# Performance work log

Hardware: AMD Instinct MI355X
Metric: run time of the kernel (lower is better)

Reference implementation:

```python
import jax, jax.numpy as jnp
import numpy as np

B, C, H, W = 16, 256, 128, 128  # ration = 1 -> C' = C


def setup_inputs() -> dict:
    key = jax.random.key(0)
    ks = jax.random.split(key, 7)
    s = 1.0 / np.sqrt(C)
    return {
        "x": jax.random.normal(ks[0], (B, C, H, W), dtype=jnp.float32),
        "Wq": jax.random.normal(ks[1], (C, C), dtype=jnp.float32) * s,
        "Wk": jax.random.normal(ks[2], (C, C), dtype=jnp.float32) * s,
        "Wv": jax.random.normal(ks[3], (C, C), dtype=jnp.float32) * s,
        "gamma": jax.random.normal(ks[4], (1,), dtype=jnp.float32) * 0.1,
        "Wup": jax.random.normal(ks[5], (C, C), dtype=jnp.float32) * s,
        "b_up": jax.random.normal(ks[6], (C,), dtype=jnp.float32) * 0.01,
    }


def reference(x, Wq, Wk, Wv, gamma, Wup, b_up):
    b, c, h, w = x.shape
    # 1x1 conv (no bias) == channel-mixing einsum, followed by ReLU
    proj = lambda Wm: jax.nn.relu(jnp.einsum('oc,bchw->bohw', Wm, x))
    # torch .view(B, H, -1) is a raw row-major reinterpretation of [B,C,H,W]
    q = proj(Wq).reshape(b, h, -1)                      # [B, H, C*W]
    k = proj(Wk).reshape(b, h, -1).transpose(0, 2, 1)   # [B, C*W, H]
    v = proj(Wv).reshape(b, h, -1).transpose(0, 2, 1)   # [B, C*W, H]
    # non-standard softmax over dim=1 (rows of the HxH score matrix)
    attn = jax.nn.softmax(jnp.matmul(q, k), axis=1)     # [B, H, H]
    out1 = jnp.matmul(v, attn)                          # [B, C*W, H]
    out_h = out1.reshape(b, c, h, w) * gamma            # raw reshape, gamma scale
    # layer_up: 1x1 conv with bias
    out_h = jnp.einsum('oc,bchw->bohw', Wup, out_h) + b_up[None, :, None, None]
    return (out_h, q, k, v, gamma, attn)
```

## Files before the change

kernel.cpp:

```cpp
#include <hip/hip_runtime.h>
#include <stdint.h>


typedef _Float16 f16;
typedef __attribute__((ext_vector_type(8))) _Float16 f16x8;
typedef __attribute__((ext_vector_type(4))) float f32x4;

#define DEV static __device__ __forceinline__

constexpr int  HW   = 16384;
constexpr long PB   = 4194304;
constexpr long HALF = 2097152;

constexpr long WH_OFF  = 0;
constexpr long WL_OFF  = 393216;
constexpr long WU_OFF  = 786432;
constexpr long WS_NEED = 1048576;

DEV unsigned pk2(float a, float b) {
  auto h = __builtin_amdgcn_cvt_pkrtz(a, b);
  return __builtin_bit_cast(unsigned, h);
}
DEV void split_pk2(float a, float b, unsigned& hu, unsigned& lu) {
  auto h = __builtin_amdgcn_cvt_pkrtz(a, b);
  auto l = __builtin_amdgcn_cvt_pkrtz(a - (float)h[0], b - (float)h[1]);
  hu = __builtin_bit_cast(unsigned, h);
  lu = __builtin_bit_cast(unsigned, l);
}
DEV f32x4 mfma16(f16x8 a, f16x8 b, f32x4 c) {
  return __builtin_amdgcn_mfma_f32_16x16x32_f16(a, b, c, 0, 0, 0);
}
DEV f16x8 ld64(const char* base, int row, int g) {
  return *(const f16x8*)(base + row * 64 + 16 * (g ^ ((row >> 1) & 3)));
}

DEV void gload16(const void* g, void* l) {
  __builtin_amdgcn_global_load_lds(
      (const __attribute__((address_space(1))) uint32_t*)(g),
      (__attribute__((address_space(3))) uint32_t*)(l), 16, 0, 0);
}

DEV int swz(int row, int kbyte) {
  return (kbyte & ~63) | ((kbyte & 63) ^ (((row >> 3) & 3) << 4));
}
DEV f16x8 ldfrag(const f16* arr, int strideB, int row, int kbyte) {
  return *(const f16x8*)((const char*)arr + row * strideB + swz(row, kbyte));
}

__global__ __launch_bounds__(256) void prep_w(
    const float* __restrict__ Wq, const float* __restrict__ Wk,
    const float* __restrict__ Wv, const float* __restrict__ Wu,
    const float* __restrict__ gin, char* __restrict__ ws) {
  const int kc = blockIdx.x, m = blockIdx.y, o = threadIdx.x;
  const float* src = (m == 0) ? Wq : (m == 1) ? Wk : (m == 2) ? Wv : Wu;
  const float sc = (m == 3) ? gin[0] : 1.0f;
  float v[32];
#pragma unroll
  for (int j = 0; j < 32; ++j) v[j] = src[o * 256 + kc * 32 + j] * sc;
  char* dh = (m < 3) ? (ws + WH_OFF + ((long)(m * 8 + kc) * 256 + o) * 64)
                     : (ws + WU_OFF + ((long)kc * 256 + o) * 64);
  char* dl = ws + WL_OFF + ((long)(m * 8 + kc) * 256 + o) * 64;
  const int sw = (o >> 1) & 3;
#pragma unroll
  for (int gq = 0; gq < 4; ++gq) {
    unsigned h[4], l[4];
#pragma unroll
    for (int p = 0; p < 4; ++p)
      split_pk2(v[8 * gq + 2 * p], v[8 * gq + 2 * p + 1], h[p], l[p]);
    const int off = 16 * (gq ^ sw);
    *(uint4*)(dh + off) = make_uint4(h[0], h[1], h[2], h[3]);
    if (m < 3) *(uint4*)(dl + off) = make_uint4(l[0], l[1], l[2], l[3]);
  }
}

__global__ __launch_bounds__(256, 2) void qkv_fused3(
    const float* __restrict__ x,
    const char* __restrict__ wqh, const char* __restrict__ wql,
    const char* __restrict__ wkh, const char* __restrict__ wkl,
    const char* __restrict__ wvh,
    float* __restrict__ qseg, float* __restrict__ kseg,
    float* __restrict__ vseg) {
  __shared__ char lds[65536];
  char* Xh = lds;
  char* Xl = lds + 32768;
  float* R = (float*)(lds + 32768);
  const int t = threadIdx.x, lane = t & 63, w = t >> 6;
  const int l15 = lane & 15, g = lane >> 4;
  const int b = blockIdx.y, hw0 = blockIdx.x * 64;
  const float* xb = x + (long)b * PB + hw0;

  {
    const int hw = t & 63, cq = t >> 6;
    const int sw = (hw >> 1) & 3;
#pragma unroll
    for (int j8 = 0; j8 < 8; ++j8) {
      const int c0 = cq * 64 + j8 * 8;
      float v[8];
#pragma unroll
      for (int i = 0; i < 8; ++i) v[i] = xb[(long)(c0 + i) * HW + hw];
      unsigned h[4], l[4];
#pragma unroll
      for (int p = 0; p < 4; ++p)
        split_pk2(v[2 * p], v[2 * p + 1], h[p], l[p]);
      const int kc = c0 >> 5, gi = (c0 >> 3) & 3;
      const int off = kc * 4096 + hw * 64 + 16 * (gi ^ sw);
      *(uint4*)(Xh + off) = make_uint4(h[0], h[1], h[2], h[3]);
      *(uint4*)(Xl + off) = make_uint4(l[0], l[1], l[2], l[3]);
    }
  }
  __syncthreads();

  auto repack_store = [&](f32x4 (&ac)[4][4], float* ob) {
#pragma unroll
    for (int half = 0; half < 2; ++half) {
#pragma unroll
      for (int mf2 = 0; mf2 < 2; ++mf2) {
        const int mf = 2 * half + mf2;
#pragma unroll
        for (int nf = 0; nf < 4; ++nf)
#pragma unroll
          for (int r = 0; r < 4; ++r) {
            const int hwloc = 16 * mf2 + 4 * g + r;
            const int o = w * 64 + 16 * nf + l15;
            const int col = (o >> 1) ^ (((hwloc >> 2) & 3) << 3);
            float v = ac[mf][nf][r];
            R[(o & 1) * 4096 + hwloc * 128 + col] = v > 0.f ? v : 0.f;
          }
      }
      __syncthreads();
#pragma unroll
      for (int it = 0; it < 8; ++it) {
        const int f = t + 256 * it;
        const int parity = f >> 10, hwloc = (f >> 5) & 31, q4 = f & 31;
        const int col = (4 * q4) ^ (((hwloc >> 2) & 3) << 3);
        const float4 v4 = *(const float4*)(R + parity * 4096 + hwloc * 128 + col);
        *(float4*)(ob + (long)parity * HALF +
                   (long)(hw0 + 32 * half + hwloc) * 128 + 4 * q4) = v4;
      }
      __syncthreads();
    }
  };

  {
    f32x4 acc[4][4] = {};
    for (int kc = 0; kc < 8; ++kc) {
      const char* XH = Xh + kc * 4096;
      const char* XL = Xl + kc * 4096;
      const char* WH = wqh + (long)kc * 16384;
      const char* WL = wql + (long)kc * 16384;
      f16x8 bh[4], bl[4];
#pragma unroll
      for (int nf = 0; nf < 4; ++nf) {
        bh[nf] = ld64(XH, 16 * nf + l15, g);
        bl[nf] = ld64(XL, 16 * nf + l15, g);
      }
#pragma unroll
      for (int mf = 0; mf < 4; ++mf) {
        const int orow = w * 64 + 16 * mf + l15;
        f16x8 ah = ld64(WH, orow, g);
        f16x8 al = ld64(WL, orow, g);
#pragma unroll
        for (int nf = 0; nf < 4; ++nf) {
          acc[mf][nf] = mfma16(ah, bh[nf], acc[mf][nf]);
          acc[mf][nf] = mfma16(ah, bl[nf], acc[mf][nf]);
          acc[mf][nf] = mfma16(al, bh[nf], acc[mf][nf]);
        }
      }
    }
    float* ob = qseg + (long)b * PB;
#pragma unroll
    for (int mf = 0; mf < 4; ++mf)
#pragma unroll
      for (int nf = 0; nf < 4; ++nf)
#pragma unroll
        for (int r = 0; r < 4; ++r) {
          float v = acc[mf][nf][r];
          v = v > 0.f ? v : 0.f;
          const int o = w * 64 + 16 * mf + 4 * g + r;
          const int hw = hw0 + 16 * nf + l15;
          ob[(long)o * HW + hw] = v;
        }
  }

  {
    f32x4 acc[4][4] = {};
    for (int kc = 0; kc < 8; ++kc) {
      const char* XH = Xh + kc * 4096;
      const char* XL = Xl + kc * 4096;
      const char* WH = wkh + (long)kc * 16384;
      const char* WL = wkl + (long)kc * 16384;
      f16x8 bh[4], bl[4];
#pragma unroll
      for (int nf = 0; nf < 4; ++nf) {
        const int orow = w * 64 + 16 * nf + l15;
        bh[nf] = ld64(WH, orow, g);
        bl[nf] = ld64(WL, orow, g);
      }
#pragma unroll
      for (int mf = 0; mf < 4; ++mf) {
        f16x8 ah = ld64(XH, 16 * mf + l15, g);
        f16x8 al = ld64(XL, 16 * mf + l15, g);
#pragma unroll
        for (int nf = 0; nf < 4; ++nf) {
          acc[mf][nf] = mfma16(ah, bh[nf], acc[mf][nf]);
          acc[mf][nf] = mfma16(ah, bl[nf], acc[mf][nf]);
          acc[mf][nf] = mfma16(al, bh[nf], acc[mf][nf]);
        }
      }
    }
    __syncthreads();
    repack_store(acc, kseg + (long)b * PB);
  }

  {
    f32x4 acc[4][4] = {};
    for (int kc = 0; kc < 8; ++kc) {
      const char* XH = Xh + kc * 4096;
      const char* WH = wvh + (long)kc * 16384;
      f16x8 bh[4];
#pragma unroll
      for (int nf = 0; nf < 4; ++nf)
        bh[nf] = ld64(WH, w * 64 + 16 * nf + l15, g);
#pragma unroll
      for (int mf = 0; mf < 4; ++mf) {
        f16x8 ah = ld64(XH, 16 * mf + l15, g);
#pragma unroll
        for (int nf = 0; nf < 4; ++nf)
          acc[mf][nf] = mfma16(ah, bh[nf], acc[mf][nf]);
      }
    }
    repack_store(acc, vseg + (long)b * PB);
  }
}

__global__ __launch_bounds__(256) void spart_kernel(
    const float* __restrict__ qseg, const float* __restrict__ kseg,
    float* __restrict__ part) {
  constexpr int SB = 80;
  __shared__ f16 Ah[128 * 40], Al[128 * 40], Bh[128 * 40], Bl[128 * 40];
  const int t = threadIdx.x, lane = t & 63, w = t >> 6;
  const int l15 = lane & 15, g = lane >> 4;
  const int ch = blockIdx.x, b = blockIdx.y;
  const float* qb = qseg + (long)b * PB + ch * 1024;
  const float* kb = kseg + (long)b * PB + (long)ch * 1024 * 128;

  f32x4 acc[4][4] = {};

  for (int kc = 0; kc < 1024; kc += 32) {
#pragma unroll
    for (int it = 0; it < 4; ++it) {
      int f4 = t + 256 * it;
      int i = f4 >> 3, c4 = f4 & 7;
      float4 v = *(const float4*)(qb + (long)i * 32768 + kc + 4 * c4);
      unsigned h01, l01, h23, l23;
      split_pk2(v.x, v.y, h01, l01);
      split_pk2(v.z, v.w, h23, l23);
      int kbo = swz(i, 8 * c4);
      *(uint2*)((char*)Ah + i * SB + kbo) = make_uint2(h01, h23);
      *(uint2*)((char*)Al + i * SB + kbo) = make_uint2(l01, l23);
    }
    {
      int c = t & 127, rh = t >> 7;
      float vs[16];
#pragma unroll
      for (int r = 0; r < 16; ++r)
        vs[r] = kb[(long)(kc + 16 * rh + r) * 128 + c];
#pragma unroll
      for (int u = 0; u < 4; ++u) {
        unsigned h0, l0, h1, l1;
        split_pk2(vs[4 * u], vs[4 * u + 1], h0, l0);
        split_pk2(vs[4 * u + 2], vs[4 * u + 3], h1, l1);
        int kbo = swz(c, 32 * rh + 8 * u);
        *(uint2*)((char*)Bh + c * SB + kbo) = make_uint2(h0, h1);
        *(uint2*)((char*)Bl + c * SB + kbo) = make_uint2(l0, l1);
      }
    }
    __syncthreads();

    f16x8 afh[4], afl[4], bfh[4], bfl[4];
#pragma unroll
    for (int f = 0; f < 4; ++f) {
      int ar = (w & 1) * 64 + 16 * f + l15;
      int br = (w >> 1) * 64 + 16 * f + l15;
      afh[f] = ldfrag(Ah, SB, ar, 16 * g);
      afl[f] = ldfrag(Al, SB, ar, 16 * g);
      bfh[f] = ldfrag(Bh, SB, br, 16 * g);
      bfl[f] = ldfrag(Bl, SB, br, 16 * g);
    }
#pragma unroll
    for (int mf = 0; mf < 4; ++mf)
#pragma unroll
      for (int nf = 0; nf < 4; ++nf) {
        acc[mf][nf] = mfma16(afh[mf], bfh[nf], acc[mf][nf]);
        acc[mf][nf] = mfma16(afh[mf], bfl[nf], acc[mf][nf]);
        acc[mf][nf] = mfma16(afl[mf], bfh[nf], acc[mf][nf]);
      }
    __syncthreads();
  }

  float* pp = part + (long)(b * 32 + ch) * 16384;
#pragma unroll
  for (int mf = 0; mf < 4; ++mf)
#pragma unroll
    for (int nf = 0; nf < 4; ++nf)
#pragma unroll
      for (int r = 0; r < 4; ++r) {
        int i = (w & 1) * 64 + 16 * mf + 4 * g + r;
        int i2 = (w >> 1) * 64 + 16 * nf + l15;
        pp[i * 128 + i2] = acc[mf][nf][r];
      }
}

__global__ __launch_bounds__(128) void reduce_s(
    const float* __restrict__ part, float* __restrict__ att,
    float* __restrict__ gout, const float* __restrict__ gin) {
  const int i = blockIdx.x, b = blockIdx.y, t = threadIdx.x;
  if (b == 0 && i == 0 && t == 0) gout[0] = gin[0];
  const float* pp = part + (long)b * 524288 + i * 128 + t;
  float s = 0.f;
#pragma unroll
  for (int c = 0; c < 32; ++c) s += pp[(long)c * 16384];
  att[((long)b * 128 + i) * 128 + t] = s;
}

__global__ __launch_bounds__(256) void softmax2(float* __restrict__ att) {
  __shared__ float red[16][17];
  const int b = blockIdx.y, c0 = blockIdx.x * 16;
  const int t = threadIdx.x, col = t & 15, ig = t >> 4;
  float* ab = att + (long)b * 16384 + c0 + col;
  float s[8];
  float m = -3.0e38f;
#pragma unroll
  for (int j = 0; j < 8; ++j) {
    s[j] = ab[(ig * 8 + j) * 128];
    m = fmaxf(m, s[j]);
  }
  red[ig][col] = m;
  __syncthreads();
  float mx = red[0][col];
#pragma unroll
  for (int k = 1; k < 16; ++k) mx = fmaxf(mx, red[k][col]);
  float sum = 0.f;
#pragma unroll
  for (int j = 0; j < 8; ++j) {
    s[j] = expf(s[j] - mx);
    sum += s[j];
  }
  __syncthreads();
  red[ig][col] = sum;
  __syncthreads();
  float tot = 0.f;
#pragma unroll
  for (int k = 0; k < 16; ++k) tot += red[k][col];
  float inv = 1.f / tot;
#pragma unroll
  for (int j = 0; j < 8; ++j) ab[(ig * 8 + j) * 128] = s[j] * inv;
}

__global__ __launch_bounds__(256, 2) void pvf_fused(
    const float* __restrict__ vseg, const float* __restrict__ att,
    const char* __restrict__ wu, const float* __restrict__ bup,
    float* __restrict__ oseg) {
  __shared__ char attnT[128 * 272];
  __shared__ char vA[64 * 272];
  __shared__ char HT[128 * 144];
  const int t = threadIdx.x, lane = t & 63, w = t >> 6;
  const int l15 = lane & 15, g = lane >> 4;
  const int b = blockIdx.y, h = blockIdx.x;
  const float* ab = att + (long)b * 16384;
  const float* vb = vseg + (long)b * PB;
  float* Ob = oseg + (long)b * PB;

#pragma unroll
  for (int it = 0; it < 4; ++it) {
    const int f = t + 256 * it;
    const int i4 = f >> 5, w4 = f & 31;
    const float4 r0 = *(const float4*)(ab + (4 * i4 + 0) * 128 + 4 * w4);
    const float4 r1 = *(const float4*)(ab + (4 * i4 + 1) * 128 + 4 * w4);
    const float4 r2 = *(const float4*)(ab + (4 * i4 + 2) * 128 + 4 * w4);
    const float4 r3 = *(const float4*)(ab + (4 * i4 + 3) * 128 + 4 * w4);
    *(uint2*)(attnT + (4 * w4 + 0) * 272 + swz(4 * w4 + 0, 8 * i4)) =
        make_uint2(pk2(r0.x, r1.x), pk2(r2.x, r3.x));
    *(uint2*)(attnT + (4 * w4 + 1) * 272 + swz(4 * w4 + 1, 8 * i4)) =
        make_uint2(pk2(r0.y, r1.y), pk2(r2.y, r3.y));
    *(uint2*)(attnT + (4 * w4 + 2) * 272 + swz(4 * w4 + 2, 8 * i4)) =
        make_uint2(pk2(r0.z, r1.z), pk2(r2.z, r3.z));
    *(uint2*)(attnT + (4 * w4 + 3) * 272 + swz(4 * w4 + 3, 8 * i4)) =
        make_uint2(pk2(r0.w, r1.w), pk2(r2.w, r3.w));
  }

  f32x4 acc2[4][8] = {};

  for (int cc = 0; cc < 4; ++cc) {
#pragma unroll
    for (int it = 0; it < 8; ++it) {
      const int f = t + 256 * it;
      const int cp = f >> 5, q4 = f & 31;
      const float4 v4 =
          *(const float4*)(vb + ((long)(cc * 64 + cp) * 128 + h) * 128 + 4 * q4);
      *(uint2*)(vA + cp * 272 + swz(cp, 8 * q4)) =
          make_uint2(pk2(v4.x, v4.y), pk2(v4.z, v4.w));
    }
    __syncthreads();

    f32x4 acc1[8] = {};
#pragma unroll
    for (int kf = 0; kf < 4; ++kf) {
      const f16x8 a = ldfrag((const f16*)vA, 272, w * 16 + l15, 64 * kf + 16 * g);
#pragma unroll
      for (int nf = 0; nf < 8; ++nf) {
        const f16x8 bf = ldfrag((const f16*)attnT, 272, 16 * nf + l15, 64 * kf + 16 * g);
        acc1[nf] = mfma16(a, bf, acc1[nf]);
      }
    }
#pragma unroll
    for (int nf = 0; nf < 8; ++nf)
#pragma unroll
      for (int r = 0; r < 4; ++r) {
        const int wp = 16 * nf + l15;
        const int cp = w * 16 + 4 * g + r;
        *(f16*)(HT + wp * 144 + swz(wp, 2 * cp)) = (f16)acc1[nf][r];
      }
    __syncthreads();

#pragma unroll
    for (int kf2 = 0; kf2 < 2; ++kf2) {
      const char* WU = wu + (long)(cc * 2 + kf2) * 16384;
      f16x8 af[4];
#pragma unroll
      for (int mf = 0; mf < 4; ++mf)
        af[mf] = ld64(WU, w * 64 + 16 * mf + l15, g);
#pragma unroll
      for (int nf = 0; nf < 8; ++nf) {
        const f16x8 bf = ldfrag((const f16*)HT, 144, 16 * nf + l15, 64 * kf2 + 16 * g);
#pragma unroll
        for (int mf = 0; mf < 4; ++mf)
          acc2[mf][nf] = mfma16(af[mf], bf, acc2[mf][nf]);
      }
    }
  }

#pragma unroll
  for (int mf = 0; mf < 4; ++mf)
#pragma unroll
    for (int nf = 0; nf < 8; ++nf)
#pragma unroll
      for (int r = 0; r < 4; ++r) {
        const int o = w * 64 + 16 * mf + 4 * g + r;
        const int wp = 16 * nf + l15;
        Ob[(long)o * HW + h * 128 + wp] = acc2[mf][nf][r] + bup[o];
      }
}

__global__ __launch_bounds__(128) void softmax_kernel(
    const float* __restrict__ part, float* __restrict__ att,
    float* __restrict__ gout, const float* __restrict__ gin) {
  const int b = blockIdx.x, t = threadIdx.x;
  if (b == 0 && t == 0) gout[0] = gin[0];
  const float* pp = part + (long)b * 32 * 16384;
  float* ab = att + (long)b * 16384;
  float mx = -3.0e38f;
  for (int i = 0; i < 128; ++i) {
    float s = 0.f;
#pragma unroll
    for (int c = 0; c < 32; ++c) s += pp[(long)c * 16384 + i * 128 + t];
    ab[i * 128 + t] = s;
    mx = fmaxf(mx, s);
  }
  float sum = 0.f;
  for (int i = 0; i < 128; ++i) {
    float e = expf(ab[i * 128 + t] - mx);
    sum += e;
    ab[i * 128 + t] = e;
  }
  float inv = 1.f / sum;
  for (int i = 0; i < 128; ++i) ab[i * 128 + t] *= inv;
}

template <int MODE>
__global__ __launch_bounds__(256) void proj_kernel(
    const float* __restrict__ x, const float* __restrict__ Wm,
    float* __restrict__ out) {
  constexpr int SB = 80;
  __shared__ f16 Wh[256 * 40];
  __shared__ f16 Wl[256 * 40];
  __shared__ f16 Xh[64 * 40];
  __shared__ f16 Xl[64 * 40];

  const int t = threadIdx.x;
  const int lane = t & 63;
  const int w = t >> 6;
  const int l15 = lane & 15;
  const int g = lane >> 4;
  const int b = blockIdx.y;
  const int hw0 = blockIdx.x * 64;
  const float* xb = x + (long)b * PB;

  f32x4 acc[4][4] = {};

  for (int kc = 0; kc < 256; kc += 32) {
#pragma unroll
    for (int it = 0; it < 8; ++it) {
      int f4 = t + 256 * it;
      int o = f4 >> 3, c4 = f4 & 7;
      float4 v = *(const float4*)(Wm + o * 256 + kc + 4 * c4);
      unsigned h01, l01, h23, l23;
      split_pk2(v.x, v.y, h01, l01);
      split_pk2(v.z, v.w, h23, l23);
      int kb = swz(o, 8 * c4);
      *(uint2*)((char*)Wh + o * SB + kb) = make_uint2(h01, h23);
      *(uint2*)((char*)Wl + o * SB + kb) = make_uint2(l01, l23);
    }
    {
      int c = t & 63, rq = t >> 6;
      float vs[8];
#pragma unroll
      for (int r = 0; r < 8; ++r)
        vs[r] = xb[(long)(kc + 8 * rq + r) * HW + hw0 + c];
#pragma unroll
      for (int u = 0; u < 2; ++u) {
        unsigned h0, l0, h1, l1;
        split_pk2(vs[4 * u], vs[4 * u + 1], h0, l0);
        split_pk2(vs[4 * u + 2], vs[4 * u + 3], h1, l1);
        int kb = swz(c, 16 * rq + 8 * u);
        *(uint2*)((char*)Xh + c * SB + kb) = make_uint2(h0, h1);
        *(uint2*)((char*)Xl + c * SB + kb) = make_uint2(l0, l1);
      }
    }
    __syncthreads();

    f16x8 wfh[4], wfl[4], xfh[4], xfl[4];
#pragma unroll
    for (int f = 0; f < 4; ++f) {
      int wr = 64 * w + 16 * f + l15;
      int xr = 16 * f + l15;
      wfh[f] = ldfrag(Wh, SB, wr, 16 * g);
      wfl[f] = ldfrag(Wl, SB, wr, 16 * g);
      xfh[f] = ldfrag(Xh, SB, xr, 16 * g);
      xfl[f] = ldfrag(Xl, SB, xr, 16 * g);
    }
#pragma unroll
    for (int mf = 0; mf < 4; ++mf)
#pragma unroll
      for (int nf = 0; nf < 4; ++nf) {
        if constexpr (MODE == 0) {
          acc[mf][nf] = mfma16(wfh[mf], xfh[nf], acc[mf][nf]);
          acc[mf][nf] = mfma16(wfh[mf], xfl[nf], acc[mf][nf]);
          acc[mf][nf] = mfma16(wfl[mf], xfh[nf], acc[mf][nf]);
        } else {
          acc[mf][nf] = mfma16(xfh[mf], wfh[nf], acc[mf][nf]);
          acc[mf][nf] = mfma16(xfh[mf], wfl[nf], acc[mf][nf]);
          acc[mf][nf] = mfma16(xfl[mf], wfh[nf], acc[mf][nf]);
        }
      }
    __syncthreads();
  }

  float* ob = out + (long)b * PB;
#pragma unroll
  for (int mf = 0; mf < 4; ++mf)
#pragma unroll
    for (int nf = 0; nf < 4; ++nf)
#pragma unroll
      for (int r = 0; r < 4; ++r) {
        float v = acc[mf][nf][r];
        v = v > 0.f ? v : 0.f;
        if constexpr (MODE == 0) {
          int o = 64 * w + 16 * mf + 4 * g + r;
          int hw = hw0 + 16 * nf + l15;
          ob[(long)o * HW + hw] = v;
        } else {
          int hw = hw0 + 16 * mf + 4 * g + r;
          int o = 64 * w + 16 * nf + l15;
          ob[((o & 1) ? HALF : 0) + (long)hw * 128 + (o >> 1)] = v;
        }
      }
}

__global__ __launch_bounds__(256) void out1_fb(
    const float* __restrict__ vseg, const float* __restrict__ att,
    float* __restrict__ outseg) {
  constexpr int SB = 272;
  __shared__ f16 Va[64 * 136], Ba[128 * 136];
  const int t = threadIdx.x, lane = t & 63, w = t >> 6;
  const int l15 = lane & 15, g = lane >> 4;
  const int b = blockIdx.y;
  const long j0 = (long)blockIdx.x * 64;
  const float* vb = vseg + (long)b * PB + j0 * 128;
  const float* ab = att + (long)b * 16384;

#pragma unroll
  for (int it = 0; it < 8; ++it) {
    int f4 = t + 256 * it;
    int j = f4 >> 5, c4 = f4 & 31;
    float4 v = *(const float4*)(vb + (long)j * 128 + 4 * c4);
    int kb = swz(j, 8 * c4);
    *(uint2*)((char*)Va + j * SB + kb) = make_uint2(pk2(v.x, v.y), pk2(v.z, v.w));
  }
  {
    int c = t & 127, rh = t >> 7;
#pragma unroll
    for (int uu = 0; uu < 16; ++uu) {
      int i0 = 64 * rh + 4 * uu;
      float v0 = ab[(i0 + 0) * 128 + c];
      float v1 = ab[(i0 + 1) * 128 + c];
      float v2 = ab[(i0 + 2) * 128 + c];
      float v3 = ab[(i0 + 3) * 128 + c];
      int kb = swz(c, 2 * i0);
      *(uint2*)((char*)Ba + c * SB + kb) = make_uint2(pk2(v0, v1), pk2(v2, v3));
    }
  }
  __syncthreads();

  f32x4 acc[2][4] = {};
#pragma unroll
  for (int kf = 0; kf < 4; ++kf) {
    f16x8 af[2], bf[4];
#pragma unroll
    for (int mf = 0; mf < 2; ++mf)
      af[mf] = ldfrag(Va, SB, (w & 1) * 32 + 16 * mf + l15, 64 * kf + 16 * g);
#pragma unroll
    for (int nf = 0; nf < 4; ++nf)
      bf[nf] = ldfrag(Ba, SB, (w >> 1) * 64 + 16 * nf + l15, 64 * kf + 16 * g);
#pragma unroll
    for (int mf = 0; mf < 2; ++mf)
#pragma unroll
      for (int nf = 0; nf < 4; ++nf)
        acc[mf][nf] = mfma16(af[mf], bf[nf], acc[mf][nf]);
  }

  float* ob = outseg + (long)b * PB;
#pragma unroll
  for (int mf = 0; mf < 2; ++mf)
#pragma unroll
    for (int nf = 0; nf < 4; ++nf)
#pragma unroll
      for (int r = 0; r < 4; ++r) {
        long j = j0 + (w & 1) * 32 + 16 * mf + 4 * g + r;
        int i2 = (w >> 1) * 64 + 16 * nf + l15;
        ob[j * 128 + i2] = acc[mf][nf][r];
      }
}

__global__ __launch_bounds__(256) void final_kernel(
    float* __restrict__ outseg, const float* __restrict__ Wup,
    const float* __restrict__ bup, const float* __restrict__ gin) {
  constexpr int SB = 144;
  __shared__ f16 Ah[256 * 72], Bh[64 * 72];
  const int t = threadIdx.x, lane = t & 63, w = t >> 6;
  const int l15 = lane & 15, g = lane >> 4;
  const int b = blockIdx.y;
  const int hw0 = blockIdx.x * 64;
  const float gamma = gin[0];
  float* Hb = outseg + (long)b * PB;

  f32x4 acc[4][4] = {};

  for (int kc = 0; kc < 256; kc += 64) {
#pragma unroll
    for (int it = 0; it < 16; ++it) {
      int f4 = t + 256 * it;
      int o = f4 >> 4, c4 = f4 & 15;
      float4 v = *(const float4*)(Wup + o * 256 + kc + 4 * c4);
      int kb = swz(o, 8 * c4);
      *(uint2*)((char*)Ah + o * SB + kb) =
          make_uint2(pk2(v.x * gamma, v.y * gamma), pk2(v.z * gamma, v.w * gamma));
    }
    {
      int n = t & 63, rq = t >> 6;
#pragma unroll
      for (int uu = 0; uu < 4; ++uu) {
        int r0 = 16 * rq + 4 * uu;
        float v0 = Hb[(long)(kc + r0 + 0) * HW + hw0 + n];
        float v1 = Hb[(long)(kc + r0 + 1) * HW + hw0 + n];
        float v2 = Hb[(long)(kc + r0 + 2) * HW + hw0 + n];
        float v3 = Hb[(long)(kc + r0 + 3) * HW + hw0 + n];
        int kb = swz(n, 2 * r0);
        *(uint2*)((char*)Bh + n * SB + kb) = make_uint2(pk2(v0, v1), pk2(v2, v3));
      }
    }
    __syncthreads();

    f16x8 af[4][2], bf[4][2];
#pragma unroll
    for (int f = 0; f < 4; ++f)
#pragma unroll
      for (int kf = 0; kf < 2; ++kf) {
        af[f][kf] = ldfrag(Ah, SB, 64 * w + 16 * f + l15, 64 * kf + 16 * g);
        bf[f][kf] = ldfrag(Bh, SB, 16 * f + l15, 64 * kf + 16 * g);
      }
#pragma unroll
    for (int mf = 0; mf < 4; ++mf)
#pragma unroll
      for (int nf = 0; nf < 4; ++nf) {
        acc[mf][nf] = mfma16(af[mf][0], bf[nf][0], acc[mf][nf]);
        acc[mf][nf] = mfma16(af[mf][1], bf[nf][1], acc[mf][nf]);
      }
    __syncthreads();
  }

#pragma unroll
  for (int mf = 0; mf < 4; ++mf)
#pragma unroll
    for (int nf = 0; nf < 4; ++nf)
#pragma unroll
      for (int r = 0; r < 4; ++r) {
        int o = 64 * w + 16 * mf + 4 * g + r;
        int hw = hw0 + 16 * nf + l15;
        Hb[(long)o * HW + hw] = acc[mf][nf][r] + bup[o];
      }
}

extern "C" void kernel_launch(void* const* d_in, const int* in_sizes, int n_in,
                              void* d_out, int out_size, void* d_ws, size_t ws_size,
                              hipStream_t stream) {
  (void)in_sizes; (void)n_in; (void)out_size;

  const float* x  = (const float*)d_in[0];
  const float* Wq = (const float*)d_in[1];
  const float* Wk = (const float*)d_in[2];
  const float* Wv = (const float*)d_in[3];
  const float* gm = (const float*)d_in[4];
  const float* Wu = (const float*)d_in[5];
  const float* bu = (const float*)d_in[6];

  float* out  = (float*)d_out;
  float* oseg = out;
  float* qseg = out + 67108864L;
  float* kseg = out + 134217728L;
  float* vseg = out + 201326592L;
  float* gseg = out + 268435456L;
  float* aseg = out + 268435457L;

  dim3 blk(256);
  if (ws_size >= (size_t)WS_NEED && d_ws != nullptr) {
    char* ws = (char*)d_ws;
    prep_w<<<dim3(8, 4), blk, 0, stream>>>(Wq, Wk, Wv, Wu, gm, ws);
    qkv_fused3<<<dim3(256, 16), blk, 0, stream>>>(
        x, ws + WH_OFF, ws + WL_OFF, ws + WH_OFF + 131072, ws + WL_OFF + 131072,
        ws + WH_OFF + 262144, qseg, kseg, vseg);
    spart_kernel<<<dim3(32, 16), blk, 0, stream>>>(qseg, kseg, oseg);
    reduce_s<<<dim3(128, 16), dim3(128), 0, stream>>>(oseg, aseg, gseg, gm);
    softmax2<<<dim3(8, 16), blk, 0, stream>>>(aseg);
    pvf_fused<<<dim3(128, 16), blk, 0, stream>>>(vseg, aseg, ws + WU_OFF, bu, oseg);
  } else {
    proj_kernel<0><<<dim3(256, 16), blk, 0, stream>>>(x, Wq, qseg);
    proj_kernel<1><<<dim3(256, 16), blk, 0, stream>>>(x, Wk, kseg);
    proj_kernel<1><<<dim3(256, 16), blk, 0, stream>>>(x, Wv, vseg);
    spart_kernel<<<dim3(32, 16), blk, 0, stream>>>(qseg, kseg, oseg);
    softmax_kernel<<<dim3(16), dim3(128), 0, stream>>>(oseg, aseg, gseg, gm);
    out1_fb<<<dim3(512, 16), blk, 0, stream>>>(vseg, aseg, oseg);
    final_kernel<<<dim3(256, 16), blk, 0, stream>>>(oseg, Wu, bu, gm);
  }
}
```

Baseline: 672.6 us.

## Load Q fragments directly to registers and double-buffer K tiles in spart

```diff
diff --git a/kernel.cpp b/kernel.cpp
--- a/kernel.cpp
+++ b/kernel.cpp
@@ -5,6 +5,7 @@
 typedef _Float16 f16;
 typedef __attribute__((ext_vector_type(8))) _Float16 f16x8;
 typedef __attribute__((ext_vector_type(4))) float f32x4;
+typedef __attribute__((ext_vector_type(4))) unsigned u32x4;
 
 #define DEV static __device__ __forceinline__
 
@@ -233,59 +234,73 @@
   }
 }
 
-__global__ __launch_bounds__(256) void spart_kernel(
+__global__ __launch_bounds__(256, 2) void spart2(
     const float* __restrict__ qseg, const float* __restrict__ kseg,
     float* __restrict__ part) {
   constexpr int SB = 80;
-  __shared__ f16 Ah[128 * 40], Al[128 * 40], Bh[128 * 40], Bl[128 * 40];
+  __shared__ f16 Bh[2][128 * 40], Bl[2][128 * 40];
   const int t = threadIdx.x, lane = t & 63, w = t >> 6;
   const int l15 = lane & 15, g = lane >> 4;
   const int ch = blockIdx.x, b = blockIdx.y;
   const float* qb = qseg + (long)b * PB + ch * 1024;
   const float* kb = kseg + (long)b * PB + (long)ch * 1024 * 128;
+  const int kc_col = t & 127, kc_rh = t >> 7;
+  const int ar0 = (w & 1) * 64, br0 = (w >> 1) * 64;
+
+  float kv[16];
+  auto loadB = [&](int kc) {
+#pragma unroll
+    for (int r = 0; r < 16; ++r)
+      kv[r] = kb[(long)(kc + 16 * kc_rh + r) * 128 + kc_col];
+  };
+  auto writeB = [&](int buf) {
+#pragma unroll
+    for (int u = 0; u < 4; ++u) {
+      unsigned h0, l0, h1, l1;
+      split_pk2(kv[4 * u], kv[4 * u + 1], h0, l0);
+      split_pk2(kv[4 * u + 2], kv[4 * u + 3], h1, l1);
+      const int kbo = swz(kc_col, 32 * kc_rh + 8 * u);
+      *(uint2*)((char*)Bh[buf] + kc_col * SB + kbo) = make_uint2(h0, h1);
+      *(uint2*)((char*)Bl[buf] + kc_col * SB + kbo) = make_uint2(l0, l1);
+    }
+  };
 
   f32x4 acc[4][4] = {};
-
-  for (int kc = 0; kc < 1024; kc += 32) {
-#pragma unroll
-    for (int it = 0; it < 4; ++it) {
-      int f4 = t + 256 * it;
-      int i = f4 >> 3, c4 = f4 & 7;
-      float4 v = *(const float4*)(qb + (long)i * 32768 + kc + 4 * c4);
-      unsigned h01, l01, h23, l23;
-      split_pk2(v.x, v.y, h01, l01);
-      split_pk2(v.z, v.w, h23, l23);
-      int kbo = swz(i, 8 * c4);
-      *(uint2*)((char*)Ah + i * SB + kbo) = make_uint2(h01, h23);
-      *(uint2*)((char*)Al + i * SB + kbo) = make_uint2(l01, l23);
-    }
-    {
-      int c = t & 127, rh = t >> 7;
-      float vs[16];
-#pragma unroll
-      for (int r = 0; r < 16; ++r)
-        vs[r] = kb[(long)(kc + 16 * rh + r) * 128 + c];
-#pragma unroll
-      for (int u = 0; u < 4; ++u) {
-        unsigned h0, l0, h1, l1;
-        split_pk2(vs[4 * u], vs[4 * u + 1], h0, l0);
-        split_pk2(vs[4 * u + 2], vs[4 * u + 3], h1, l1);
-        int kbo = swz(c, 32 * rh + 8 * u);
-        *(uint2*)((char*)Bh + c * SB + kbo) = make_uint2(h0, h1);
-        *(uint2*)((char*)Bl + c * SB + kbo) = make_uint2(l0, l1);
-      }
-    }
-    __syncthreads();
-
-    f16x8 afh[4], afl[4], bfh[4], bfl[4];
+  loadB(0);
+  writeB(0);
+  __syncthreads();
+
+  for (int s = 0; s < 32; ++s) {
+    const int kc = s * 32;
+    f32x4 av[4][2];
+#pragma unroll
+    for (int mf = 0; mf < 4; ++mf) {
+      const float* src = qb + (long)(ar0 + 16 * mf + l15) * 32768 + kc + 8 * g;
+      av[mf][0] = *(const f32x4*)src;
+      av[mf][1] = *(const f32x4*)(src + 4);
+    }
+    if (s < 31) loadB(kc + 32);
+
+    f16x8 afh[4], afl[4];
+#pragma unroll
+    for (int mf = 0; mf < 4; ++mf) {
+      unsigned h0, l0, h1, l1, h2, l2, h3, l3;
+      split_pk2(av[mf][0][0], av[mf][0][1], h0, l0);
+      split_pk2(av[mf][0][2], av[mf][0][3], h1, l1);
+      split_pk2(av[mf][1][0], av[mf][1][1], h2, l2);
+      split_pk2(av[mf][1][2], av[mf][1][3], h3, l3);
+      u32x4 uh = {h0, h1, h2, h3};
+      u32x4 ul = {l0, l1, l2, l3};
+      afh[mf] = __builtin_bit_cast(f16x8, uh);
+      afl[mf] = __builtin_bit_cast(f16x8, ul);
+    }
+    const f16* BH = Bh[s & 1];
+    const f16* BL = Bl[s & 1];
+    f16x8 bfh[4], bfl[4];
 #pragma unroll
     for (int f = 0; f < 4; ++f) {
-      int ar = (w & 1) * 64 + 16 * f + l15;
-      int br = (w >> 1) * 64 + 16 * f + l15;
-      afh[f] = ldfrag(Ah, SB, ar, 16 * g);
-      afl[f] = ldfrag(Al, SB, ar, 16 * g);
-      bfh[f] = ldfrag(Bh, SB, br, 16 * g);
-      bfl[f] = ldfrag(Bl, SB, br, 16 * g);
+      bfh[f] = ldfrag(BH, SB, br0 + 16 * f + l15, 16 * g);
+      bfl[f] = ldfrag(BL, SB, br0 + 16 * f + l15, 16 * g);
     }
 #pragma unroll
     for (int mf = 0; mf < 4; ++mf)
@@ -295,6 +310,8 @@
         acc[mf][nf] = mfma16(afh[mf], bfl[nf], acc[mf][nf]);
         acc[mf][nf] = mfma16(afl[mf], bfh[nf], acc[mf][nf]);
       }
+
+    if (s < 31) writeB((s + 1) & 1);
     __syncthreads();
   }
 
@@ -305,8 +322,8 @@
     for (int nf = 0; nf < 4; ++nf)
 #pragma unroll
       for (int r = 0; r < 4; ++r) {
-        int i = (w & 1) * 64 + 16 * mf + 4 * g + r;
-        int i2 = (w >> 1) * 64 + 16 * nf + l15;
+        int i = ar0 + 16 * mf + 4 * g + r;
+        int i2 = br0 + 16 * nf + l15;
         pp[i * 128 + i2] = acc[mf][nf][r];
       }
 }
@@ -739,7 +756,7 @@
     qkv_fused3<<<dim3(256, 16), blk, 0, stream>>>(
         x, ws + WH_OFF, ws + WL_OFF, ws + WH_OFF + 131072, ws + WL_OFF + 131072,
         ws + WH_OFF + 262144, qseg, kseg, vseg);
-    spart_kernel<<<dim3(32, 16), blk, 0, stream>>>(qseg, kseg, oseg);
+    spart2<<<dim3(32, 16), blk, 0, stream>>>(qseg, kseg, oseg);
     reduce_s<<<dim3(128, 16), dim3(128), 0, stream>>>(oseg, aseg, gseg, gm);
     softmax2<<<dim3(8, 16), blk, 0, stream>>>(aseg);
     pvf_fused<<<dim3(128, 16), blk, 0, stream>>>(vseg, aseg, ws + WU_OFF, bu, oseg);
@@ -747,7 +764,7 @@
     proj_kernel<0><<<dim3(256, 16), blk, 0, stream>>>(x, Wq, qseg);
     proj_kernel<1><<<dim3(256, 16), blk, 0, stream>>>(x, Wk, kseg);
     proj_kernel<1><<<dim3(256, 16), blk, 0, stream>>>(x, Wv, vseg);
-    spart_kernel<<<dim3(32, 16), blk, 0, stream>>>(qseg, kseg, oseg);
+    spart2<<<dim3(32, 16), blk, 0, stream>>>(qseg, kseg, oseg);
     softmax_kernel<<<dim3(16), dim3(128), 0, stream>>>(oseg, aseg, gseg, gm);
     out1_fb<<<dim3(512, 16), blk, 0, stream>>>(vseg, aseg, oseg);
     final_kernel<<<dim3(256, 16), blk, 0, stream>>>(oseg, Wu, bu, gm);
```

Result: no change. 679.6 us (+1.0%).
